# Kernel tuning notes

Measured on AMD Instinct MI355X. Metric: run time of the kernel, lower is better.

Reference implementation:

```python
import jax, jax.numpy as jnp
import numpy as np

# ---- config (from repo's config module, standard values) ----
GH, GW = 32, 64            # control grid
FULL_H, FULL_W = 128, 512  # target_image (n_mels, frames)
N_FFT, HOP = 1024, 256
N_FREQ = N_FFT // 2 + 1    # 513
N_ITER, MOMENTUM = 32, 0.99
NUM_SAMPLES = 131072
BATCH = 8

# periodic hann window (torch.hann_window default)
_WIN = 0.5 * (1.0 - jnp.cos(2.0 * jnp.pi * jnp.arange(N_FFT) / N_FFT))


def _stft(x):
    # x: (B, L) -> (B, N_FREQ, F); center=True reflect pad, hann window
    pad = N_FFT // 2
    xp = jnp.pad(x, ((0, 0), (pad, pad)), mode='reflect')
    n_frames = 1 + (xp.shape[-1] - N_FFT) // HOP
    idx = jnp.arange(n_frames)[:, None] * HOP + jnp.arange(N_FFT)[None, :]
    frames = xp[:, idx] * _WIN  # (B, F, N_FFT)
    return jnp.fft.rfft(frames, axis=-1).transpose(0, 2, 1)  # (B, N_FREQ, F)


def _istft(S, length):
    # S: (B, N_FREQ, F) -> (B, length); windowed overlap-add, center trim
    frames = jnp.fft.irfft(S.transpose(0, 2, 1), n=N_FFT, axis=-1) * _WIN  # (B,F,N_FFT)
    B, F, _ = frames.shape
    total = N_FFT + HOP * (F - 1)
    idx = (jnp.arange(F)[:, None] * HOP + jnp.arange(N_FFT)[None, :]).reshape(-1)
    sig = jnp.zeros((B, total), frames.dtype).at[:, idx].add(frames.reshape(B, -1))
    wsq = jnp.zeros((total,), frames.dtype).at[idx].add(jnp.tile(_WIN ** 2, F))
    sig = sig / jnp.where(wsq > 1e-11, wsq, 1.0)
    pad = N_FFT // 2
    return sig[:, pad:pad + length]


def _griffin_lim(spec_power):
    # spec_power: (B, N_FREQ, W) power spectrogram (power=2.0)
    mag = jnp.sqrt(jnp.maximum(spec_power, 0.0))
    W = spec_power.shape[-1]
    length = HOP * (W - 1)
    # random unit-magnitude initial phase (torchaudio rand_init)
    u = jax.random.uniform(jax.random.key(1), mag.shape, dtype=jnp.float32)
    angles = jnp.exp(1j * (2.0 * jnp.pi) * u).astype(jnp.complex64)
    tprev = jnp.zeros_like(angles)
    for _ in range(N_ITER):  # fixed 32 iterations
        inverse = _istft(mag.astype(jnp.complex64) * angles, length)
        rebuilt = _stft(inverse)
        angles = rebuilt - tprev * (MOMENTUM / (1.0 + MOMENTUM))
        angles = angles / (jnp.abs(angles) + 1e-16)
        tprev = rebuilt
    return _istft(mag.astype(jnp.complex64) * angles, length)  # (B, length)


def setup_inputs() -> dict:
    key = jax.random.key(0)
    params = jax.random.uniform(key, (BATCH, GH * GW), dtype=jnp.float32)
    return {"params": params}


def reference(params):
    B = params.shape[0]
    grid = params.reshape(B, GH, GW)
    # F.interpolate(..., mode='bilinear', align_corners=False) == jax.image.resize bilinear
    full_spec = jax.image.resize(grid, (B, FULL_H, FULL_W), method='bilinear')  # (B,H,W)
    spec_power = full_spec ** 2 * 100.0
    linear_spec = jax.image.resize(spec_power, (B, N_FREQ, FULL_W), method='bilinear')
    audio = _griffin_lim(linear_spec)  # (B, (W-1)*HOP)
    # pad/trim to NUM_SAMPLES
    L = audio.shape[-1]
    if L < NUM_SAMPLES:
        audio = jnp.pad(audio, ((0, 0), (0, NUM_SAMPLES - L)))
    else:
        audio = audio[:, :NUM_SAMPLES]
    max_val = jnp.maximum(jnp.max(jnp.abs(audio), axis=-1, keepdims=True), 1e-8)
    audio = audio / max_val * 0.9
    return audio, full_spec
```

## Files before the change

### kernel.cpp

```cpp
#include <hip/hip_runtime.h>

typedef unsigned int u32;

constexpr int BATCH = 8;
constexpr int GH = 32, GW = 64;
constexpr int FH = 128, FW = 512;
constexpr int NFFT = 1024;
constexpr int HOP = 256;
constexpr int NFREQ = 513;
constexpr int NW = 512;
constexpr int SIGLEN = HOP * (NW - 1);
constexpr int TOTAL_LEN = NFFT + HOP*(NW-1);
constexpr int NITER = 32;
constexpr int NSAMP = 131072;
constexpr int NMAG = BATCH * NW * NFREQ;

#define SL(i) ((i) + ((i) >> 3))
constexpr int WSL = 576;
constexpr int XSPAN = 4 * HOP + (NFFT - HOP);

#define WAVEFENCE() __builtin_amdgcn_wave_barrier()

__device__ __forceinline__ void tf_round(u32 &x0, u32 &x1, int r) {
  x0 += x1;
  x1 = (x1 << r) | (x1 >> (32 - r));
  x1 ^= x0;
}

__device__ __forceinline__ void threefry2(u32 c0, u32 c1, u32 &o0, u32 &o1) {
  const u32 k0 = 0u, k1 = 1u;
  const u32 k2 = 0x1BD11BDAu ^ k0 ^ k1;
  u32 x0 = c0 + k0, x1 = c1 + k1;
  tf_round(x0, x1, 13); tf_round(x0, x1, 15); tf_round(x0, x1, 26); tf_round(x0, x1, 6);
  x0 += k1; x1 += k2 + 1u;
  tf_round(x0, x1, 17); tf_round(x0, x1, 29); tf_round(x0, x1, 16); tf_round(x0, x1, 24);
  x0 += k2; x1 += k0 + 2u;
  tf_round(x0, x1, 13); tf_round(x0, x1, 15); tf_round(x0, x1, 26); tf_round(x0, x1, 6);
  x0 += k0; x1 += k1 + 3u;
  tf_round(x0, x1, 17); tf_round(x0, x1, 29); tf_round(x0, x1, 16); tf_round(x0, x1, 24);
  x0 += k1; x1 += k2 + 4u;
  tf_round(x0, x1, 13); tf_round(x0, x1, 15); tf_round(x0, x1, 26); tf_round(x0, x1, 6);
  x0 += k2; x1 += k0 + 5u;
  o0 = x0; o1 = x1;
}

__global__ __launch_bounds__(256) void k_init(float* __restrict__ win,
                                              float2* __restrict__ tw512f, double2* __restrict__ twh,
                                              float* __restrict__ wsq,
                                              float2* __restrict__ tprev)
{
  int idx = blockIdx.x * 256 + threadIdx.x;
  int stride = gridDim.x * 256;
  const double PI2 = 6.283185307179586476925286766559;
  for (int t = idx; t < NFFT; t += stride)
    win[t] = (float)(0.5 * (1.0 - cos(PI2 * (double)t / 1024.0)));
  for (int k = idx; k < 512; k += stride) {
    double th = -PI2 * (double)k / 512.0;
    tw512f[k] = make_float2((float)cos(th), (float)sin(th));
    double th2 = -PI2 * (double)k / 1024.0;
    double2 v2; v2.x = cos(th2); v2.y = sin(th2);
    twh[k] = v2;
  }
  for (int j = idx; j < TOTAL_LEN; j += stride) {
    int gmax = j >> 8; if (gmax > NW - 1) gmax = NW - 1;
    int gmin = (j >= NFFT) ? ((j - (NFFT - 1) + 255) >> 8) : 0;
    float acc = 0.f;
    for (int g = gmin; g <= gmax; ++g) {
      float w = (float)(0.5 * (1.0 - cos(PI2 * (double)(j - (g << 8)) / 1024.0)));
      acc = __fadd_rn(acc, __fmul_rn(w, w));
    }
    wsq[j] = acc;
  }
  for (int i = idx; i < NMAG; i += stride)
    tprev[i] = make_float2(0.f, 0.f);
}

__device__ __forceinline__ void lin_taps(float sf, int in, int &i0, int &i1, float &w0, float &w1)
{
  if (sf <= 0.0f)                  { i0 = 0;      i1 = 0;      w0 = 1.0f; w1 = 0.0f; return; }
  if (sf >= (float)(in - 1))       { i0 = in - 1; i1 = in - 1; w0 = 1.0f; w1 = 0.0f; return; }
  i0 = (int)sf; i1 = i0 + 1;
  float x0 = __fsub_rn(sf, (float)i0);
  float a0 = __fsub_rn(1.0f, x0);
  float S  = __fadd_rn(a0, x0);
  w0 = __fdiv_rn(a0, S);
  w1 = __fdiv_rn(x0, S);
}

__device__ __forceinline__ float sf_H1(int H) {
  return __fadd_rn(__fmul_rn(__fadd_rn((float)H, 0.5f), 0.25f), -0.5f);
}
__device__ __forceinline__ float sf_W1(int W) {
  return __fadd_rn(__fmul_rn(__fadd_rn((float)W, 0.5f), 0.125f), -0.5f);
}
__device__ __forceinline__ float sf_H2(int K) {
  const float inv32 = (float)(1.0 / 4.0078125);
  return __fadd_rn(__fmul_rn(__fadd_rn((float)K, 0.5f), inv32), -0.5f);
}

__device__ __forceinline__ float fs_at(const float* __restrict__ pb, int H, int W)
{
  int r0, r1; float u0, u1;
  lin_taps(sf_H1(H), GH, r0, r1, u0, u1);
  int c0, c1; float v0, v1;
  lin_taps(sf_W1(W), GW, c0, c1, v0, v1);
  float t0 = __fmaf_rn(u1, pb[r1 * GW + c0], __fmul_rn(u0, pb[r0 * GW + c0]));
  float t1 = __fmaf_rn(u1, pb[r1 * GW + c1], __fmul_rn(u0, pb[r0 * GW + c1]));
  return __fmaf_rn(v1, t1, __fmul_rn(v0, t0));
}

__global__ __launch_bounds__(256) void k_fullspec(const float* __restrict__ p, float* __restrict__ fs)
{
  int idx = blockIdx.x * 256 + threadIdx.x;
  if (idx >= BATCH * FH * FW) return;
  int b = idx >> 16;
  int h = (idx >> 9) & (FH - 1);
  int w = idx & (FW - 1);
  fs[idx] = fs_at(p + b * (GH * GW), h, w);
}

__global__ __launch_bounds__(256) void k_mag(const float* __restrict__ p, float* __restrict__ mag)
{
  int idx = blockIdx.x * 256 + threadIdx.x;
  if (idx >= NMAG) return;
  int b = idx / (NW * NFREQ);
  int rem = idx - b * (NW * NFREQ);
  int f = rem / NFREQ;
  int k = rem - f * NFREQ;
  const float* pb = p + b * (GH * GW);
  int h0, h1; float wa, wb;
  lin_taps(sf_H2(k), FH, h0, h1, wa, wb);
  float fs0 = fs_at(pb, h0, f);
  float fs1 = fs_at(pb, h1, f);
  float P0 = __fmul_rn(__fmul_rn(fs0, fs0), 100.0f);
  float P1 = __fmul_rn(__fmul_rn(fs1, fs1), 100.0f);
  float lin = __fmaf_rn(wb, P1, __fmul_rn(wa, P0));
  mag[idx] = __fsqrt_rn(fmaxf(lin, 0.0f));
}

__global__ __launch_bounds__(256) void k_phase(float2* __restrict__ ang)
{
  int idx = blockIdx.x * 256 + threadIdx.x;
  if (idx >= NMAG) return;
  int b = idx / (NW * NFREQ);
  int rem = idx - b * (NW * NFREQ);
  int f = rem / NFREQ;
  int k = rem - f * NFREQ;
  u32 cnt = (u32)(b * (NFREQ * NW) + k * NW + f);
  u32 w0, w1;
  threefry2(0u, cnt, w0, w1);
  u32 bits = w0 ^ w1;
  float u = __uint_as_float((bits >> 9) | 0x3f800000u) - 1.0f;
  float th = __fmul_rn((float)6.283185307179586, u);
  double thd = (double)th;
  ang[idx] = make_float2((float)cos(thd), (float)sin(thd));
}

__device__ __forceinline__ float2 cadd2(float2 a, float2 b){ return make_float2(a.x+b.x, a.y+b.y); }
__device__ __forceinline__ float2 csub2(float2 a, float2 b){ return make_float2(a.x-b.x, a.y-b.y); }

template<bool INV>
__device__ __forceinline__ float2 twmul(float2 a, float2 w)
{
  float wy = INV ? -w.y : w.y;
  return make_float2(a.x*w.x - a.y*wy, a.x*wy + a.y*w.x);
}

template<bool INV>
__device__ __forceinline__ void bfly8(float2 x0, float2 x1, float2 x2, float2 x3,
                                      float2 x4, float2 x5, float2 x6, float2 x7,
                                      float2 &Y0, float2 &Y1, float2 &Y2, float2 &Y3,
                                      float2 &Y4, float2 &Y5, float2 &Y6, float2 &Y7)
{
  const float c = 0.70710678118654752440f;
  float2 u0 = cadd2(x0,x4), u1 = cadd2(x1,x5), u2 = cadd2(x2,x6), u3 = cadd2(x3,x7);
  float2 d0 = csub2(x0,x4), d1 = csub2(x1,x5), d2 = csub2(x2,x6), d3 = csub2(x3,x7);
  float2 w1, w2, w3;
  if (!INV) {
    w1 = make_float2(c*(d1.x + d1.y), c*(d1.y - d1.x));
    w2 = make_float2(d2.y, -d2.x);
    w3 = make_float2(c*(d3.y - d3.x), -c*(d3.x + d3.y));
  } else {
    w1 = make_float2(c*(d1.x - d1.y), c*(d1.x + d1.y));
    w2 = make_float2(-d2.y, d2.x);
    w3 = make_float2(-c*(d3.x + d3.y), c*(d3.x - d3.y));
  }
  float2 s0 = cadd2(u0,u2), s1 = cadd2(u1,u3), s2 = csub2(u0,u2);
  float2 e13 = csub2(u1,u3);
  float2 s3 = INV ? make_float2(-e13.y, e13.x) : make_float2(e13.y, -e13.x);
  float2 r0 = cadd2(d0,w2), r1 = cadd2(w1,w3), r2 = csub2(d0,w2);
  float2 e57 = csub2(w1,w3);
  float2 r3 = INV ? make_float2(-e57.y, e57.x) : make_float2(e57.y, -e57.x);
  Y0 = cadd2(s0,s1); Y4 = csub2(s0,s1);
  Y2 = cadd2(s2,s3); Y6 = csub2(s2,s3);
  Y1 = cadd2(r0,r1); Y5 = csub2(r0,r1);
  Y3 = cadd2(r2,r3); Y7 = csub2(r2,r3);
}

template<bool INV>
__device__ __forceinline__ void stage0_regs(float2* __restrict__ A, const float2* __restrict__ tw, int t,
    float2 x0, float2 x1, float2 x2, float2 x3, float2 x4, float2 x5, float2 x6, float2 x7)
{
  float2 Y0,Y1,Y2,Y3,Y4,Y5,Y6,Y7;
  bfly8<INV>(x0,x1,x2,x3,x4,x5,x6,x7, Y0,Y1,Y2,Y3,Y4,Y5,Y6,Y7);
  int ob = 8 * t;
  A[SL(ob + 0)] = Y0;
  A[SL(ob + 1)] = twmul<INV>(Y1, tw[t]);
  A[SL(ob + 2)] = twmul<INV>(Y2, tw[2 * t]);
  A[SL(ob + 3)] = twmul<INV>(Y3, tw[3 * t]);
  A[SL(ob + 4)] = twmul<INV>(Y4, tw[4 * t]);
  A[SL(ob + 5)] = twmul<INV>(Y5, tw[5 * t]);
  A[SL(ob + 6)] = twmul<INV>(Y6, tw[6 * t]);
  A[SL(ob + 7)] = twmul<INV>(Y7, tw[7 * t]);
}

template<bool INV>
__device__ __forceinline__ void stage_mid(float2* __restrict__ A, const float2* __restrict__ tw, int t)
{
  float2 x0 = A[SL(t)],       x1 = A[SL(t + 64)],  x2 = A[SL(t + 128)], x3 = A[SL(t + 192)];
  float2 x4 = A[SL(t + 256)], x5 = A[SL(t + 320)], x6 = A[SL(t + 384)], x7 = A[SL(t + 448)];
  float2 Y0,Y1,Y2,Y3,Y4,Y5,Y6,Y7;
  bfly8<INV>(x0,x1,x2,x3,x4,x5,x6,x7, Y0,Y1,Y2,Y3,Y4,Y5,Y6,Y7);
  WAVEFENCE();
  int p = t >> 3, q = t & 7;
  int base = 8 * p;
  int ob = q + 64 * p;
  A[SL(ob)]      = Y0;
  A[SL(ob + 8)]  = twmul<INV>(Y1, tw[base]);
  A[SL(ob + 16)] = twmul<INV>(Y2, tw[2 * base]);
  A[SL(ob + 24)] = twmul<INV>(Y3, tw[3 * base]);
  A[SL(ob + 32)] = twmul<INV>(Y4, tw[4 * base]);
  A[SL(ob + 40)] = twmul<INV>(Y5, tw[5 * base]);
  A[SL(ob + 48)] = twmul<INV>(Y6, tw[6 * base]);
  A[SL(ob + 56)] = twmul<INV>(Y7, tw[7 * base]);
}

template<bool INV>
__device__ __forceinline__ void stage_last_lds(float2* __restrict__ A, int t)
{
  float2 x0 = A[SL(t)],       x1 = A[SL(t + 64)],  x2 = A[SL(t + 128)], x3 = A[SL(t + 192)];
  float2 x4 = A[SL(t + 256)], x5 = A[SL(t + 320)], x6 = A[SL(t + 384)], x7 = A[SL(t + 448)];
  float2 Y0,Y1,Y2,Y3,Y4,Y5,Y6,Y7;
  bfly8<INV>(x0,x1,x2,x3,x4,x5,x6,x7, Y0,Y1,Y2,Y3,Y4,Y5,Y6,Y7);
  WAVEFENCE();
  A[SL(t)]       = Y0; A[SL(t + 64)]  = Y1; A[SL(t + 128)] = Y2; A[SL(t + 192)] = Y3;
  A[SL(t + 256)] = Y4; A[SL(t + 320)] = Y5; A[SL(t + 384)] = Y6; A[SL(t + 448)] = Y7;
}

template<bool INV>
__device__ __forceinline__ void stage_last_regs(const float2* __restrict__ A, int t,
    float2 &Y0, float2 &Y1, float2 &Y2, float2 &Y3, float2 &Y4, float2 &Y5, float2 &Y6, float2 &Y7)
{
  float2 x0 = A[SL(t)],       x1 = A[SL(t + 64)],  x2 = A[SL(t + 128)], x3 = A[SL(t + 192)];
  float2 x4 = A[SL(t + 256)], x5 = A[SL(t + 320)], x6 = A[SL(t + 384)], x7 = A[SL(t + 448)];
  bfly8<INV>(x0,x1,x2,x3,x4,x5,x6,x7, Y0,Y1,Y2,Y3,Y4,Y5,Y6,Y7);
}

__device__ __forceinline__ void upd_bin(float2* __restrict__ prow, float2* __restrict__ A,
                                        int k, double rx, double ry, float cf)
{
  float rxf = (float)rx, ryf = (float)ry;
  float2 pv = prow[k];
  float ax = __fsub_rn(rxf, __fmul_rn(pv.x, cf));
  float ay = __fsub_rn(ryf, __fmul_rn(pv.y, cf));
  double dx = (double)ax, dy = (double)ay;
  float d = (float)sqrt(dx * dx + dy * dy);
  float d2 = __fadd_rn(d, 1e-16f);
  float inv = __fdiv_rn(1.0f, d2);
  int slot = (k == 512) ? (WSL - 1) : SL(k);
  A[slot] = make_float2(__fmul_rn(ax, inv), __fmul_rn(ay, inv));
  prow[k] = make_float2(rxf, ryf);
}

__global__ __launch_bounds__(256) void k_istft(const float* __restrict__ mag, const float2* __restrict__ ang,
                                               float* __restrict__ frames,
                                               const float2* __restrict__ tw512f,
                                               const double2* __restrict__ twh,
                                               const float* __restrict__ win)
{
  __shared__ float2 ldsA[4 * WSL];
  __shared__ float2 twl[512];
  int tid = threadIdx.x;
  for (int i = tid; i < 512; i += 256) twl[i] = tw512f[i];
  __syncthreads();

  int wv = tid >> 6;
  int t  = tid & 63;
  int bf = (blockIdx.x << 2) + wv;
  float2* A = ldsA + wv * WSL;
  const float*  mrow = mag + bf * NFREQ;
  const float2* arow = ang + bf * NFREQ;

  float2 z0, z1, z2, z3, z4, z5, z6, z7;
#define PACKG(j, zj) { \
    int k = t + 64 * j; \
    if (k == 0) { \
      float m1 = mrow[0];   float2 a1 = arow[0]; \
      float m2 = mrow[512]; float2 a2 = arow[512]; \
      float S1x = __fmul_rn(m1, a1.x); \
      float S2x = __fmul_rn(m2, a2.x); \
      zj = make_float2((float)(0.5 * ((double)S1x + (double)S2x)), \
                       (float)(0.5 * ((double)S1x - (double)S2x))); \
    } else { \
      int k2 = 512 - k; \
      float m1 = mrow[k];  float2 a1 = arow[k]; \
      float m2 = mrow[k2]; float2 a2 = arow[k2]; \
      float S1x = __fmul_rn(m1, a1.x), S1y = __fmul_rn(m1, a1.y); \
      float S2x = __fmul_rn(m2, a2.x), S2y = __fmul_rn(m2, a2.y); \
      double Xex = 0.5 * ((double)S1x + (double)S2x); \
      double Xey = 0.5 * ((double)S1y - (double)S2y); \
      double Dx  = 0.5 * ((double)S1x - (double)S2x); \
      double Dy  = 0.5 * ((double)S1y + (double)S2y); \
      double2 w = twh[k]; \
      double ux = w.x * Dx + w.y * Dy; \
      double uy = w.x * Dy - w.y * Dx; \
      zj = make_float2((float)(Xex - uy), (float)(Xey + ux)); \
    } }
  PACKG(0, z0) PACKG(1, z1) PACKG(2, z2) PACKG(3, z3)
  PACKG(4, z4) PACKG(5, z5) PACKG(6, z6) PACKG(7, z7)

  stage0_regs<true>(A, twl, t, z0, z1, z2, z3, z4, z5, z6, z7);
  WAVEFENCE();
  stage_mid<true>(A, twl, t);
  WAVEFENCE();
  float2 y0, y1, y2, y3, y4, y5, y6, y7;
  stage_last_regs<true>(A, t, y0, y1, y2, y3, y4, y5, y6, y7);

  const float sc = 1.0f / 512.0f;
  const float2* win2 = (const float2*)win;
  float2* frow2 = (float2*)(frames + bf * NFFT);
#define STOREF(k, yk) { int m = t + 64 * k; float2 wv2 = win2[m]; \
    frow2[m] = make_float2(__fmul_rn(__fmul_rn(yk.x, sc), wv2.x), \
                           __fmul_rn(__fmul_rn(yk.y, sc), wv2.y)); }
  STOREF(0, y0) STOREF(1, y1) STOREF(2, y2) STOREF(3, y3)
  STOREF(4, y4) STOREF(5, y5) STOREF(6, y6) STOREF(7, y7)
}

__device__ __forceinline__ float sig_sample(const float* __restrict__ fb, const float* __restrict__ wsq, int j)
{
  int gmax = j >> 8; if (gmax > NW - 1) gmax = NW - 1;
  int gmin = (j >= NFFT) ? ((j - (NFFT - 1) + 255) >> 8) : 0;
  float acc = 0.f;
  for (int g = gmin; g <= gmax; ++g)
    acc = __fadd_rn(acc, fb[g * NFFT + (j - (g << 8))]);
  float wv = wsq[j];
  return __fdiv_rn(acc, wv > 1e-11f ? wv : 1.0f);
}

__global__ __launch_bounds__(256) void k_fused(const float* __restrict__ frames_in,
                                               const float* __restrict__ wsq,
                                               const float* __restrict__ win,
                                               const float2* __restrict__ tw512f,
                                               const double2* __restrict__ twh,
                                               const float* __restrict__ mag,
                                               float2* __restrict__ tprev,
                                               float* __restrict__ frames_out)
{
  __shared__ float2 ldsA[4 * WSL];
  __shared__ float2 twl[512];
  __shared__ float2 xpL2[XSPAN / 2];
  float* xpL = (float*)xpL2;
  int tid = threadIdx.x;
  for (int i = tid; i < 512; i += 256) twl[i] = tw512f[i];

  int bf0 = blockIdx.x << 2;
  int b  = bf0 >> 9;
  int f0 = bf0 & (NW - 1);
  const float* fb = frames_in + b * (NW * NFFT);
  int xbase = f0 * HOP;
#pragma unroll
  for (int c = 0; c < XSPAN / 256; ++c) {
    int s = tid + 256 * c;
    int j = xbase + s;
    int n = j - 512;
    if (n < 0) n = -n;
    if (n >= SIGLEN) n = 2 * SIGLEN - 2 - n;
    xpL[s] = sig_sample(fb, wsq, n + 512);
  }
  __syncthreads();

  int wv = tid >> 6;
  int t  = tid & 63;
  int bf = bf0 + wv;
  float2* A = ldsA + wv * WSL;
  const float2* win2 = (const float2*)win;

  const float2* xrow2 = (const float2*)(xpL + wv * HOP);
  float2 x0, x1, x2, x3, x4, x5, x6, x7;
#define LOADX(j, xj) { float2 xv = xrow2[t + 64 * j]; float2 wv2 = win2[t + 64 * j]; \
    xj = make_float2(__fmul_rn(xv.x, wv2.x), __fmul_rn(xv.y, wv2.y)); }
  LOADX(0, x0) LOADX(1, x1) LOADX(2, x2) LOADX(3, x3)
  LOADX(4, x4) LOADX(5, x5) LOADX(6, x6) LOADX(7, x7)
  stage0_regs<false>(A, twl, t, x0, x1, x2, x3, x4, x5, x6, x7);
  WAVEFENCE();
  stage_mid<false>(A, twl, t);
  WAVEFENCE();
  stage_last_lds<false>(A, t);
  WAVEFENCE();

  float2* prow = tprev + bf * NFREQ;
  const float cf = (float)(0.99 / 1.99);
#pragma unroll
  for (int j = 0; j < 4; ++j) {
    int k = t + 64 * j;
    if (k == 0) {
      float2 Z0 = A[SL(0)];
      double rx0 = (double)Z0.x + (double)Z0.y;
      double rx5 = (double)Z0.x - (double)Z0.y;
      upd_bin(prow, A, 0,   rx0, 0.0, cf);
      upd_bin(prow, A, 512, rx5, 0.0, cf);
    } else {
      int kc = 512 - k;
      float2 Zk = A[SL(k)];
      float2 Zc = A[SL(kc)];
      double Xex = 0.5 * ((double)Zk.x + (double)Zc.x);
      double Xey = 0.5 * ((double)Zk.y - (double)Zc.y);
      double Gx  = 0.5 * ((double)Zk.x - (double)Zc.x);
      double Gy  = 0.5 * ((double)Zk.y + (double)Zc.y);
      double2 w = twh[k];
      double P = w.x * Gy + w.y * Gx;
      double Q = w.y * Gy - w.x * Gx;
      upd_bin(prow, A, k,  Xex + P, Xey + Q, cf);
      upd_bin(prow, A, kc, Xex - P, Q - Xey, cf);
    }
  }
  if (t == 0) {
    float2 Zk = A[SL(256)];
    double Xex = 0.5 * ((double)Zk.x + (double)Zk.x);
    double Gy  = 0.5 * ((double)Zk.y + (double)Zk.y);
    double2 w = twh[256];
    double P = w.x * Gy;
    double Q = w.y * Gy;
    upd_bin(prow, A, 256, Xex + P, Q, cf);
  }
  WAVEFENCE();

  const float* mrow = mag + bf * NFREQ;
  float2 z0, z1, z2, z3, z4, z5, z6, z7;
#define PACKL(j, zj) { \
    int k = t + 64 * j; \
    if (k == 0) { \
      float m1 = mrow[0];   float2 a1 = A[SL(0)]; \
      float m2 = mrow[512]; float2 a2 = A[WSL - 1]; \
      float S1x = __fmul_rn(m1, a1.x); \
      float S2x = __fmul_rn(m2, a2.x); \
      zj = make_float2((float)(0.5 * ((double)S1x + (double)S2x)), \
                       (float)(0.5 * ((double)S1x - (double)S2x))); \
    } else { \
      int k2 = 512 - k; \
      float m1 = mrow[k];  float2 a1 = A[SL(k)]; \
      float m2 = mrow[k2]; float2 a2 = A[SL(k2)]; \
      float S1x = __fmul_rn(m1, a1.x), S1y = __fmul_rn(m1, a1.y); \
      float S2x = __fmul_rn(m2, a2.x), S2y = __fmul_rn(m2, a2.y); \
      double Xex = 0.5 * ((double)S1x + (double)S2x); \
      double Xey = 0.5 * ((double)S1y - (double)S2y); \
      double Dx  = 0.5 * ((double)S1x - (double)S2x); \
      double Dy  = 0.5 * ((double)S1y + (double)S2y); \
      double2 w = twh[k]; \
      double ux = w.x * Dx + w.y * Dy; \
      double uy = w.x * Dy - w.y * Dx; \
      zj = make_float2((float)(Xex - uy), (float)(Xey + ux)); \
    } }
  PACKL(0, z0) PACKL(1, z1) PACKL(2, z2) PACKL(3, z3)
  PACKL(4, z4) PACKL(5, z5) PACKL(6, z6) PACKL(7, z7)
  WAVEFENCE();

  stage0_regs<true>(A, twl, t, z0, z1, z2, z3, z4, z5, z6, z7);
  WAVEFENCE();
  stage_mid<true>(A, twl, t);
  WAVEFENCE();
  float2 y0, y1, y2, y3, y4, y5, y6, y7;
  stage_last_regs<true>(A, t, y0, y1, y2, y3, y4, y5, y6, y7);

  const float sc = 1.0f / 512.0f;
  float2* frow2 = (float2*)(frames_out + bf * NFFT);
  STOREF(0, y0) STOREF(1, y1) STOREF(2, y2) STOREF(3, y3)
  STOREF(4, y4) STOREF(5, y5) STOREF(6, y6) STOREF(7, y7)
}

__global__ __launch_bounds__(256) void k_ola(const float* __restrict__ frames, const float* __restrict__ wsq,
                                             float* __restrict__ audio, float* __restrict__ partial)
{
  int idx = blockIdx.x * 256 + threadIdx.x;
  int b  = idx >> 17;
  int nn = idx & (NSAMP - 1);
  float v = 0.f;
  if (nn < SIGLEN)
    v = sig_sample(frames + b * (NW * NFFT), wsq, nn + 512);
  audio[idx] = v;
  __shared__ float red[256];
  red[threadIdx.x] = fabsf(v);
  __syncthreads();
  for (int s = 128; s > 0; s >>= 1) {
    if (threadIdx.x < s) red[threadIdx.x] = fmaxf(red[threadIdx.x], red[threadIdx.x + s]);
    __syncthreads();
  }
  if (threadIdx.x == 0) partial[blockIdx.x] = red[0];
}

constexpr int OLA_BLK_PER_B = NSAMP / 256;

__global__ __launch_bounds__(256) void k_max2(const float* __restrict__ partial, float* __restrict__ maxbuf)
{
  int b = blockIdx.x;
  float m = 0.f;
  for (int i = threadIdx.x; i < OLA_BLK_PER_B; i += 256)
    m = fmaxf(m, partial[b * OLA_BLK_PER_B + i]);
  __shared__ float red[256];
  red[threadIdx.x] = m;
  __syncthreads();
  for (int s = 128; s > 0; s >>= 1) {
    if (threadIdx.x < s) red[threadIdx.x] = fmaxf(red[threadIdx.x], red[threadIdx.x + s]);
    __syncthreads();
  }
  if (threadIdx.x == 0) maxbuf[b] = red[0];
}

__global__ __launch_bounds__(256) void k_norm(const float* __restrict__ audio, const float* __restrict__ maxbuf,
                                              float* __restrict__ out)
{
  int idx = blockIdx.x * 256 + threadIdx.x;
  int b = idx >> 17;
  float m = fmaxf(maxbuf[b], 1e-8f);
  out[idx] = __fmul_rn(__fdiv_rn(audio[idx], m), 0.9f);
}

extern "C" void kernel_launch(void* const* d_in, const int* in_sizes, int n_in,
                              void* d_out, int out_size, void* d_ws, size_t ws_size,
                              hipStream_t stream)
{
  const float* params = (const float*)d_in[0];
  float* out   = (float*)d_out;
  float* audio_out = out;
  float* fs        = out + BATCH * NSAMP;

  float2*  tw512f = (float2*)d_ws;
  double2* twh    = (double2*)(tw512f + 512);
  float2*  ang    = (float2*)(twh + 512);
  float2*  tprev  = ang + NMAG;
  float*   framesA= (float*)(tprev + NMAG);
  float*   mag    = framesA + BATCH * NW * NFFT;
  float*   win    = mag + NMAG;
  float*   wsq    = win + NFFT;
  float*   audio32= wsq + TOTAL_LEN;
  float*   maxbuf = audio32 + BATCH * NSAMP;
  float*   partial= maxbuf + BATCH;
  float*   framesB= (float*)ang;

  k_init<<<512, 256, 0, stream>>>(win, tw512f, twh, wsq, tprev);
  k_fullspec<<<(BATCH * FH * FW) / 256, 256, 0, stream>>>(params, fs);
  k_mag<<<(NMAG + 255) / 256, 256, 0, stream>>>(params, mag);
  k_phase<<<(NMAG + 255) / 256, 256, 0, stream>>>(ang);

  k_istft<<<BATCH * NW / 4, 256, 0, stream>>>(mag, (const float2*)ang, framesA, tw512f, twh, win);
  float* fin  = framesA;
  float* fout = framesB;
  for (int it = 0; it < NITER; ++it) {
    k_fused<<<BATCH * NW / 4, 256, 0, stream>>>(fin, wsq, win, tw512f, twh, mag, tprev, fout);
    float* tmp = fin; fin = fout; fout = tmp;
  }
  k_ola<<<(BATCH * NSAMP) / 256, 256, 0, stream>>>(fin, wsq, audio32, partial);
  k_max2<<<BATCH, 256, 0, stream>>>(partial, maxbuf);
  k_norm<<<(BATCH * NSAMP) / 256, 256, 0, stream>>>(audio32, maxbuf, audio_out);
}
```

Before: 926.8 us.

## Fuse Griffin-Lim iterations into one persistent cooperative kernel with grid barriers

Replaces the 32 separate k_fused launches with a single cooperatively launched persistent kernel that loops over the iterations and synchronizes through a two-level atomic grid barrier. The momentum state (tprev) and magnitude values are kept in registers across iterations instead of being reloaded from and written back to global memory. This targets per-launch overhead and global traffic for tprev and mag, at the cost of barrier spin latency and a requirement that all 1024 blocks be co-resident. If the cooperative launch fails, it falls back to the old launch loop.

```diff
diff --git a/kernel.cpp b/kernel.cpp
--- a/kernel.cpp
+++ b/kernel.cpp
@@ -14,6 +14,8 @@
 constexpr int NITER = 32;
 constexpr int NSAMP = 131072;
 constexpr int NMAG = BATCH * NW * NFREQ;
+constexpr int NBLK = BATCH * NW / 4;
+constexpr int NGRP = 32;
 
 #define SL(i) ((i) + ((i) >> 3))
 constexpr int WSL = 576;
@@ -47,7 +49,8 @@
 __global__ __launch_bounds__(256) void k_init(float* __restrict__ win,
                                               float2* __restrict__ tw512f, double2* __restrict__ twh,
                                               float* __restrict__ wsq,
-                                              float2* __restrict__ tprev)
+                                              float2* __restrict__ tprev,
+                                              u32* __restrict__ bar)
 {
   int idx = blockIdx.x * 256 + threadIdx.x;
   int stride = gridDim.x * 256;
@@ -73,6 +76,8 @@
   }
   for (int i = idx; i < NMAG; i += stride)
     tprev[i] = make_float2(0.f, 0.f);
+  for (int i = idx; i < NITER * (NGRP + 1); i += stride)
+    bar[i] = 0u;
 }
 
 __device__ __forceinline__ void lin_taps(float sf, int in, int &i0, int &i1, float &w0, float &w1)
@@ -270,6 +275,20 @@
   int slot = (k == 512) ? (WSL - 1) : SL(k);
   A[slot] = make_float2(__fmul_rn(ax, inv), __fmul_rn(ay, inv));
   prow[k] = make_float2(rxf, ryf);
+}
+
+__device__ __forceinline__ void upd_reg(float2 &tprev, float2* __restrict__ A,
+                                        int slot, double rx, double ry, float cf)
+{
+  float rxf = (float)rx, ryf = (float)ry;
+  float ax = __fsub_rn(rxf, __fmul_rn(tprev.x, cf));
+  float ay = __fsub_rn(ryf, __fmul_rn(tprev.y, cf));
+  double dx = (double)ax, dy = (double)ay;
+  float d = (float)sqrt(dx * dx + dy * dy);
+  float d2 = __fadd_rn(d, 1e-16f);
+  float inv = __fdiv_rn(1.0f, d2);
+  A[slot] = make_float2(__fmul_rn(ax, inv), __fmul_rn(ay, inv));
+  tprev = make_float2(rxf, ryf);
 }
 
 __global__ __launch_bounds__(256) void k_istft(const float* __restrict__ mag, const float2* __restrict__ ang,
@@ -387,10 +406,10 @@
 
   const float2* xrow2 = (const float2*)(xpL + wv * HOP);
   float2 x0, x1, x2, x3, x4, x5, x6, x7;
-#define LOADX(j, xj) { float2 xv = xrow2[t + 64 * j]; float2 wv2 = win2[t + 64 * j]; \
+#define LOADXF(j, xj) { float2 xv = xrow2[t + 64 * j]; float2 wv2 = win2[t + 64 * j]; \
     xj = make_float2(__fmul_rn(xv.x, wv2.x), __fmul_rn(xv.y, wv2.y)); }
-  LOADX(0, x0) LOADX(1, x1) LOADX(2, x2) LOADX(3, x3)
-  LOADX(4, x4) LOADX(5, x5) LOADX(6, x6) LOADX(7, x7)
+  LOADXF(0, x0) LOADXF(1, x1) LOADXF(2, x2) LOADXF(3, x3)
+  LOADXF(4, x4) LOADXF(5, x5) LOADXF(6, x6) LOADXF(7, x7)
   stage0_regs<false>(A, twl, t, x0, x1, x2, x3, x4, x5, x6, x7);
   WAVEFENCE();
   stage_mid<false>(A, twl, t);
@@ -437,7 +456,7 @@
 
   const float* mrow = mag + bf * NFREQ;
   float2 z0, z1, z2, z3, z4, z5, z6, z7;
-#define PACKL(j, zj) { \
+#define PACKLF(j, zj) { \
     int k = t + 64 * j; \
     if (k == 0) { \
       float m1 = mrow[0];   float2 a1 = A[SL(0)]; \
@@ -461,8 +480,8 @@
       double uy = w.x * Dy - w.y * Dx; \
       zj = make_float2((float)(Xex - uy), (float)(Xey + ux)); \
     } }
-  PACKL(0, z0) PACKL(1, z1) PACKL(2, z2) PACKL(3, z3)
-  PACKL(4, z4) PACKL(5, z5) PACKL(6, z6) PACKL(7, z7)
+  PACKLF(0, z0) PACKLF(1, z1) PACKLF(2, z2) PACKLF(3, z3)
+  PACKLF(4, z4) PACKLF(5, z5) PACKLF(6, z6) PACKLF(7, z7)
   WAVEFENCE();
 
   stage0_regs<true>(A, twl, t, z0, z1, z2, z3, z4, z5, z6, z7);
@@ -476,6 +495,175 @@
   float2* frow2 = (float2*)(frames_out + bf * NFFT);
   STOREF(0, y0) STOREF(1, y1) STOREF(2, y2) STOREF(3, y3)
   STOREF(4, y4) STOREF(5, y5) STOREF(6, y6) STOREF(7, y7)
+}
+
+__device__ __forceinline__ void grid_barrier(u32* __restrict__ grp, u32* __restrict__ root, int it)
+{
+  __syncthreads();
+  if (threadIdx.x == 0) {
+    __threadfence();
+    int g = (int)(blockIdx.x >> 5);
+    if (atomicAdd(&grp[it * NGRP + g], 1u) == 31u) {
+      __threadfence();
+      atomicAdd(&root[it], 1u);
+    }
+    while (__hip_atomic_load(&root[it], __ATOMIC_RELAXED, __HIP_MEMORY_SCOPE_AGENT) < (u32)NGRP)
+      __builtin_amdgcn_s_sleep(2);
+    __threadfence();
+  }
+  __syncthreads();
+}
+
+__global__ __launch_bounds__(256, 4) void k_loop(float* __restrict__ framesA,
+                                                 float* __restrict__ framesB,
+                                                 const float* __restrict__ wsq,
+                                                 const float* __restrict__ win,
+                                                 const float2* __restrict__ tw512f,
+                                                 const double2* __restrict__ twh,
+                                                 const float* __restrict__ mag,
+                                                 u32* __restrict__ grp,
+                                                 u32* __restrict__ root)
+{
+  __shared__ float2 ldsA[4 * WSL];
+  __shared__ float2 twl[512];
+  __shared__ float2 xpL2[XSPAN / 2];
+  float* xpL = (float*)xpL2;
+
+  int tid = threadIdx.x;
+  int wv = tid >> 6;
+  int t  = tid & 63;
+  int bf0 = blockIdx.x << 2;
+  int b  = bf0 >> 9;
+  int f0 = bf0 & (NW - 1);
+  int bf = bf0 + wv;
+  float2* A = ldsA + wv * WSL;
+  const float2* win2 = (const float2*)win;
+
+  for (int i = tid; i < 512; i += 256) twl[i] = tw512f[i];
+
+  const float* mrow = mag + bf * NFREQ;
+  float mg0 = mrow[t],       mg1 = mrow[t + 64],  mg2 = mrow[t + 128], mg3 = mrow[t + 192];
+  float mg4 = mrow[t + 256], mg5 = mrow[t + 320], mg6 = mrow[t + 384], mg7 = mrow[t + 448];
+  float mh0 = mrow[512 - t], mh1 = mrow[448 - t], mh2 = mrow[384 - t], mh3 = mrow[320 - t];
+  float mh4 = mrow[256 - t], mh5 = mrow[192 - t], mh6 = mrow[128 - t], mh7 = mrow[64 - t];
+
+  float2 tp0 = make_float2(0.f, 0.f), tp1 = tp0, tp2 = tp0, tp3 = tp0;
+  float2 tq0 = tp0, tq1 = tp0, tq2 = tp0, tq3 = tp0;
+  float2 tr  = tp0;
+
+  const float cf = (float)(0.99 / 1.99);
+  const float sc = 1.0f / 512.0f;
+  int xbase = f0 * HOP;
+
+  for (int it = 0; it < NITER; ++it) {
+    const float* fin  = (it & 1) ? framesB : framesA;
+    float*       fout = (it & 1) ? framesA : framesB;
+    const float* fb = fin + b * (NW * NFFT);
+
+#pragma unroll
+    for (int c = 0; c < XSPAN / 256; ++c) {
+      int s = tid + 256 * c;
+      int j = xbase + s;
+      int n = j - 512;
+      if (n < 0) n = -n;
+      if (n >= SIGLEN) n = 2 * SIGLEN - 2 - n;
+      xpL[s] = sig_sample(fb, wsq, n + 512);
+    }
+    __syncthreads();
+
+    const float2* xrow2 = (const float2*)(xpL + wv * HOP);
+    float2 x0, x1, x2, x3, x4, x5, x6, x7;
+#define LOADX2(j, xj) { float2 xv = xrow2[t + 64 * j]; float2 wv2 = win2[t + 64 * j]; \
+    xj = make_float2(__fmul_rn(xv.x, wv2.x), __fmul_rn(xv.y, wv2.y)); }
+    LOADX2(0, x0) LOADX2(1, x1) LOADX2(2, x2) LOADX2(3, x3)
+    LOADX2(4, x4) LOADX2(5, x5) LOADX2(6, x6) LOADX2(7, x7)
+    stage0_regs<false>(A, twl, t, x0, x1, x2, x3, x4, x5, x6, x7);
+    WAVEFENCE();
+    stage_mid<false>(A, twl, t);
+    WAVEFENCE();
+    stage_last_lds<false>(A, t);
+    WAVEFENCE();
+
+#define UPDP2(j, tpj, tqj) { \
+      int k = t + 64 * (j); \
+      if ((j) == 0 && k == 0) { \
+        float2 Z0 = A[SL(0)]; \
+        double rx0 = (double)Z0.x + (double)Z0.y; \
+        double rx5 = (double)Z0.x - (double)Z0.y; \
+        upd_reg(tpj, A, SL(0),   rx0, 0.0, cf); \
+        upd_reg(tqj, A, WSL - 1, rx5, 0.0, cf); \
+      } else { \
+        int kc = 512 - k; \
+        float2 Zk = A[SL(k)]; \
+        float2 Zc = A[SL(kc)]; \
+        double Xex = 0.5 * ((double)Zk.x + (double)Zc.x); \
+        double Xey = 0.5 * ((double)Zk.y - (double)Zc.y); \
+        double Gx  = 0.5 * ((double)Zk.x - (double)Zc.x); \
+        double Gy  = 0.5 * ((double)Zk.y + (double)Zc.y); \
+        double2 w = twh[k]; \
+        double P = w.x * Gy + w.y * Gx; \
+        double Q = w.y * Gy - w.x * Gx; \
+        upd_reg(tpj, A, SL(k),  Xex + P, Xey + Q, cf); \
+        upd_reg(tqj, A, SL(kc), Xex - P, Q - Xey, cf); \
+      } }
+    UPDP2(0, tp0, tq0)
+    UPDP2(1, tp1, tq1)
+    UPDP2(2, tp2, tq2)
+    UPDP2(3, tp3, tq3)
+    if (t == 0) {
+      float2 Zk = A[SL(256)];
+      double Xex = 0.5 * ((double)Zk.x + (double)Zk.x);
+      double Gy  = 0.5 * ((double)Zk.y + (double)Zk.y);
+      double2 w = twh[256];
+      double P = w.x * Gy;
+      double Q = w.y * Gy;
+      upd_reg(tr, A, SL(256), Xex + P, Q, cf);
+    }
+    WAVEFENCE();
+
+    float2 z0, z1, z2, z3, z4, z5, z6, z7;
+#define PACKL2(j, zj, mgj, mhj) { \
+      int k = t + 64 * j; \
+      if (k == 0) { \
+        float2 a1 = A[SL(0)]; \
+        float2 a2 = A[WSL - 1]; \
+        float S1x = __fmul_rn(mgj, a1.x); \
+        float S2x = __fmul_rn(mhj, a2.x); \
+        zj = make_float2((float)(0.5 * ((double)S1x + (double)S2x)), \
+                         (float)(0.5 * ((double)S1x - (double)S2x))); \
+      } else { \
+        int k2 = 512 - k; \
+        float2 a1 = A[SL(k)]; \
+        float2 a2 = A[SL(k2)]; \
+        float S1x = __fmul_rn(mgj, a1.x), S1y = __fmul_rn(mgj, a1.y); \
+        float S2x = __fmul_rn(mhj, a2.x), S2y = __fmul_rn(mhj, a2.y); \
+        double Xex = 0.5 * ((double)S1x + (double)S2x); \
+        double Xey = 0.5 * ((double)S1y - (double)S2y); \
+        double Dx  = 0.5 * ((double)S1x - (double)S2x); \
+        double Dy  = 0.5 * ((double)S1y + (double)S2y); \
+        double2 w = twh[k]; \
+        double ux = w.x * Dx + w.y * Dy; \
+        double uy = w.x * Dy - w.y * Dx; \
+        zj = make_float2((float)(Xex - uy), (float)(Xey + ux)); \
+      } }
+    PACKL2(0, z0, mg0, mh0) PACKL2(1, z1, mg1, mh1) PACKL2(2, z2, mg2, mh2) PACKL2(3, z3, mg3, mh3)
+    PACKL2(4, z4, mg4, mh4) PACKL2(5, z5, mg5, mh5) PACKL2(6, z6, mg6, mh6) PACKL2(7, z7, mg7, mh7)
+    WAVEFENCE();
+
+    stage0_regs<true>(A, twl, t, z0, z1, z2, z3, z4, z5, z6, z7);
+    WAVEFENCE();
+    stage_mid<true>(A, twl, t);
+    WAVEFENCE();
+    float2 y0, y1, y2, y3, y4, y5, y6, y7;
+    stage_last_regs<true>(A, t, y0, y1, y2, y3, y4, y5, y6, y7);
+
+    float2* frow2 = (float2*)(fout + bf * NFFT);
+    STOREF(0, y0) STOREF(1, y1) STOREF(2, y2) STOREF(3, y3)
+    STOREF(4, y4) STOREF(5, y5) STOREF(6, y6) STOREF(7, y7)
+
+    if (it != NITER - 1)
+      grid_barrier(grp, root, it);
+  }
 }
 
 __global__ __launch_bounds__(256) void k_ola(const float* __restrict__ frames, const float* __restrict__ wsq,
@@ -545,21 +733,32 @@
   float*   audio32= wsq + TOTAL_LEN;
   float*   maxbuf = audio32 + BATCH * NSAMP;
   float*   partial= maxbuf + BATCH;
+  u32*     bar    = (u32*)(partial + BATCH * OLA_BLK_PER_B);
+  u32*     grpbar = bar;
+  u32*     rootbar= bar + NITER * NGRP;
   float*   framesB= (float*)ang;
 
-  k_init<<<512, 256, 0, stream>>>(win, tw512f, twh, wsq, tprev);
+  k_init<<<512, 256, 0, stream>>>(win, tw512f, twh, wsq, tprev, bar);
   k_fullspec<<<(BATCH * FH * FW) / 256, 256, 0, stream>>>(params, fs);
   k_mag<<<(NMAG + 255) / 256, 256, 0, stream>>>(params, mag);
   k_phase<<<(NMAG + 255) / 256, 256, 0, stream>>>(ang);
 
-  k_istft<<<BATCH * NW / 4, 256, 0, stream>>>(mag, (const float2*)ang, framesA, tw512f, twh, win);
-  float* fin  = framesA;
-  float* fout = framesB;
-  for (int it = 0; it < NITER; ++it) {
-    k_fused<<<BATCH * NW / 4, 256, 0, stream>>>(fin, wsq, win, tw512f, twh, mag, tprev, fout);
-    float* tmp = fin; fin = fout; fout = tmp;
-  }
-  k_ola<<<(BATCH * NSAMP) / 256, 256, 0, stream>>>(fin, wsq, audio32, partial);
+  k_istft<<<NBLK, 256, 0, stream>>>(mag, (const float2*)ang, framesA, tw512f, twh, win);
+
+  void* args[] = { (void*)&framesA, (void*)&framesB, (void*)&wsq, (void*)&win,
+                   (void*)&tw512f, (void*)&twh, (void*)&mag,
+                   (void*)&grpbar, (void*)&rootbar };
+  hipError_t ce = hipLaunchCooperativeKernel((const void*)k_loop, dim3(NBLK), dim3(256),
+                                             args, 0, stream);
+  if (ce != hipSuccess) {
+    float* fin  = framesA;
+    float* fout = framesB;
+    for (int it = 0; it < NITER; ++it) {
+      k_fused<<<NBLK, 256, 0, stream>>>(fin, wsq, win, tw512f, twh, mag, tprev, fout);
+      float* tmp = fin; fin = fout; fout = tmp;
+    }
+  }
+  k_ola<<<(BATCH * NSAMP) / 256, 256, 0, stream>>>(framesA, wsq, audio32, partial);
   k_max2<<<BATCH, 256, 0, stream>>>(partial, maxbuf);
   k_norm<<<(BATCH * NSAMP) / 256, 256, 0, stream>>>(audio32, maxbuf, audio_out);
 }
```

Measured after the change: 3.158 ms. +240.7%, slower.
